# Performance work log

Measured on AMD Instinct MI355X. Metric: run time of the kernel, lower is better.

## Reference

```python
import jax, jax.numpy as jnp
import numpy as np

E = 1024
H = 16          # num_heads
D = E // H      # head_dim
HID = 1024      # hidden_dim
B, S = 16, 512
EPS = 1e-5


def _ln(x, g, b):
    mu = jnp.mean(x, axis=-1, keepdims=True)
    var = jnp.mean(jnp.square(x - mu), axis=-1, keepdims=True)
    return (x - mu) * jax.lax.rsqrt(var + EPS) * g + b


def setup_inputs() -> dict:
    key = jax.random.key(0)
    ks = jax.random.split(key, 8)
    s = 1.0 / np.sqrt(E)
    return {
        'state_features': jax.random.normal(ks[0], (6, B, S, E), jnp.float32),
        'Wq': jax.random.normal(ks[1], (E, E), jnp.float32) * s,
        'bq': jnp.zeros((E,), jnp.float32),
        'Wk': jax.random.normal(ks[2], (E, E), jnp.float32) * s,
        'bk': jnp.zeros((E,), jnp.float32),
        'Wv': jax.random.normal(ks[3], (E, E), jnp.float32) * s,
        'bv': jnp.zeros((E,), jnp.float32),
        'Wo': jax.random.normal(ks[4], (E, E), jnp.float32) * s,
        'bo': jnp.zeros((E,), jnp.float32),
        'ln1_g': jnp.ones((E,), jnp.float32),
        'ln1_b': jnp.zeros((E,), jnp.float32),
        'fusion_w': jnp.ones((6,), jnp.float32) / 6.0,
        'Wf': jax.random.normal(ks[5], (HID, E), jnp.float32) * s,
        'bf': jnp.zeros((HID,), jnp.float32),
        'ln2_g': jnp.ones((HID,), jnp.float32),
        'ln2_b': jnp.zeros((HID,), jnp.float32),
    }


def reference(state_features, Wq, bq, Wk, bk, Wv, bv, Wo, bo,
              ln1_g, ln1_b, fusion_w, Wf, bf, ln2_g, ln2_b):
    # state_features: (6, B, S, E) -> stacked (N, 6, E), N = B*S
    st = jnp.transpose(state_features, (1, 2, 0, 3)).reshape(B * S, 6, E)
    N = st.shape[0]

    q = (st @ Wq.T + bq).reshape(N, 6, H, D)
    k = (st @ Wk.T + bk).reshape(N, 6, H, D)
    v = (st @ Wv.T + bv).reshape(N, 6, H, D)

    # tiny 6x6 attention per token per head (dropout = identity in eval)
    scores = jnp.einsum('nqhd,nkhd->nhqk', q, k) / np.sqrt(D).astype(np.float32)
    attn = jax.nn.softmax(scores, axis=-1)
    ctx = jnp.einsum('nhqk,nkhd->nqhd', attn, v).reshape(N, 6, E)

    out = ctx @ Wo.T + bo
    enhanced = _ln(out + st, ln1_g, ln1_b)  # (N, 6, E)

    # weighted_sum fusion
    w = jax.nn.softmax(fusion_w)
    fused = jnp.einsum('nse,s->ne', enhanced, w)

    hidden = fused @ Wf.T + bf
    hidden = jnp.where(hidden >= 0, hidden, 0.01 * hidden)  # LeakyReLU(0.01)
    hidden = _ln(hidden, ln2_g, ln2_b)
    return hidden.reshape(B, S, HID)
```

## Files before the change

### kernel.cpp

```cpp
#include <hip/hip_runtime.h>
#include <hip/hip_bf16.h>

#define NTOK 8192
#define E 1024
#define NS 6
#define MBIG (NTOK * NS)
#define NSE ((long)NTOK * E)

typedef short short8 __attribute__((ext_vector_type(8)));
typedef float f32x4 __attribute__((ext_vector_type(4)));
typedef unsigned short ushort4v __attribute__((ext_vector_type(4)));

#define TM 128
#define TN 128
#define BK 64

static __device__ __forceinline__ float bf2f(unsigned short u) {
    union { unsigned int i; float f; } c; c.i = ((unsigned int)u) << 16; return c.f;
}

struct WPtrs { const float* s[5]; __hip_bfloat16* d[5]; };
__global__ __launch_bounds__(256) void cvt5_w(WPtrs p)
{
    const int seg = blockIdx.x >> 10;
    const int i = ((blockIdx.x & 1023) * 256 + threadIdx.x) * 4;
    const float4 v = *(const float4*)(p.s[seg] + i);
    union { __hip_bfloat16 h[4]; unsigned long long u; } pk;
    pk.h[0] = (__hip_bfloat16)v.x;
    pk.h[1] = (__hip_bfloat16)v.y;
    pk.h[2] = (__hip_bfloat16)v.z;
    pk.h[3] = (__hip_bfloat16)v.w;
    *(unsigned long long*)(p.d[seg] + i) = pk.u;
}

__global__ __launch_bounds__(256) void cvt_bulk(
    const float* __restrict__ src, __hip_bfloat16* __restrict__ dst)
{
    const long i = ((long)blockIdx.x * 256 + threadIdx.x) * 4;
    const float4 v = *(const float4*)(src + i);
    union { __hip_bfloat16 h[4]; unsigned long long u; } pk;
    pk.h[0] = (__hip_bfloat16)v.x;
    pk.h[1] = (__hip_bfloat16)v.y;
    pk.h[2] = (__hip_bfloat16)v.z;
    pk.h[3] = (__hip_bfloat16)v.w;
    *(unsigned long long*)(dst + i) = pk.u;
}

#define KTILES 16
#define NITER  8

static __device__ __forceinline__ void stage_half(
    const __hip_bfloat16* gsrc,
    __hip_bfloat16* ldst, int tid)
{
#pragma unroll
    for (int piece = 0; piece < 2; ++piece) {
        const int r  = piece * 64 + (tid >> 3);
        const int s  = tid & 7;
        const int ss = s ^ (r & 7);
        const __hip_bfloat16* g = gsrc + (long)r * 1024 + ss * 8;
        __hip_bfloat16* l = ldst + r * 64 + s * 8;
        __builtin_amdgcn_global_load_lds((const __attribute__((address_space(1))) void*)g,
                                         (__attribute__((address_space(3))) void*)l, 16, 0, 0);
    }
}

static __device__ __forceinline__ short8 ld_frag(
    const __hip_bfloat16* half_base, int lr, int slot)
{
    return *(const short8*)(half_base + lr * 64 + ((slot ^ (lr & 7)) << 3));
}

#define STAGE(kt, part)                                                         \
  {                                                                             \
    const int _b  = (kt) & 1;                                                   \
    const int _ab = (part) >> 1;                                                \
    const int _hf = (part) & 1;                                                 \
    const __hip_bfloat16* _g = (_ab == 0)                                       \
        ? A  + (m0 + _hf * 128) * 1024 + (kt) * 64                              \
        : Wb + ((long)n0 + _hf * 128) * 1024 + (kt) * 64;                       \
    stage_half(_g, &lds[((_b * 2 + _ab) * 2 + _hf) * 8192], tid);               \
  }

#define PHASE(kt, q, STMT_STAGE, STMT_WAIT)                                     \
  {                                                                             \
    const int _buf = (kt) & 1;                                                  \
    const __hip_bfloat16* _Ab = &lds[((_buf * 2 + 0) * 2 + wm) * 8192];         \
    const __hip_bfloat16* _Bb = &lds[((_buf * 2 + 1) * 2 + (wn >> 1)) * 8192];  \
    if ((q) == 0) {                                                             \
      _Pragma("unroll") for (int nf = 0; nf < 4; ++nf)                          \
        _Pragma("unroll") for (int k2 = 0; k2 < 2; ++k2)                        \
          bfr[nf][k2] = ld_frag(_Bb, (wn & 1) * 64 + nf * 16 + mrow,            \
                                k2 * 4 + quad);                                 \
    }                                                                           \
    _Pragma("unroll") for (int mf = 0; mf < 2; ++mf)                            \
      _Pragma("unroll") for (int k2 = 0; k2 < 2; ++k2)                          \
        afr[mf][k2] = ld_frag(_Ab, (q) * 32 + mf * 16 + mrow, k2 * 4 + quad);   \
    STMT_STAGE;                                                                 \
    STMT_WAIT;                                                                  \
    __builtin_amdgcn_s_barrier();                                               \
    asm volatile("s_waitcnt lgkmcnt(0)" ::: "memory");                          \
    __builtin_amdgcn_sched_barrier(0);                                          \
    __builtin_amdgcn_s_setprio(1);                                              \
    _Pragma("unroll") for (int mf = 0; mf < 2; ++mf)                            \
      _Pragma("unroll") for (int nf = 0; nf < 4; ++nf)                          \
        _Pragma("unroll") for (int k2 = 0; k2 < 2; ++k2)                        \
          acc[(q) * 2 + mf][nf] = __builtin_amdgcn_mfma_f32_16x16x32_bf16(      \
              afr[mf][k2], bfr[nf][k2], acc[(q) * 2 + mf][nf], 0, 0, 0);        \
    __builtin_amdgcn_s_setprio(0);                                              \
    __builtin_amdgcn_s_barrier();                                               \
  }

__global__ __launch_bounds__(512) void gemm256(
    const __hip_bfloat16* __restrict__ A,
    const __hip_bfloat16* __restrict__ Wb,
    const float* __restrict__ bias,
    __hip_bfloat16* __restrict__ C)
{
    __shared__ __hip_bfloat16 lds[2 * 2 * 2 * 8192] __attribute__((aligned(16)));

    const int tid  = threadIdx.x;
    const int lane = tid & 63;
    const int wid  = tid >> 6;
    const int quad = lane >> 4;
    const int mrow = lane & 15;
    const int wm = wid >> 2;
    const int wn = wid & 3;

    const int nwg = gridDim.x * gridDim.y;
    const int cpx = nwg >> 3;
    const int lin = blockIdx.y * gridDim.x + blockIdx.x;
    const int tile = (lin & 7) * cpx + (lin >> 3);
    const int  n0 = (tile & 3) * 256;
    const long m0 = (long)(tile >> 2) * 256;

    f32x4 acc[8][4] = {};
    short8 bfr[4][2];
    short8 afr[2][2];

    STAGE(0, 0); STAGE(0, 1); STAGE(0, 2); STAGE(0, 3);
    STAGE(1, 2); STAGE(1, 3);
    asm volatile("s_waitcnt vmcnt(4)" ::: "memory");
    __builtin_amdgcn_s_barrier();

#pragma unroll 1
    for (int it = 0; it < NITER; ++it) {
        const int kt0 = 2 * it;
        const int kt1 = 2 * it + 1;
        const bool more = (it < NITER - 1);

        PHASE(kt0, 0, STAGE(kt1, 0), ((void)0));
        PHASE(kt0, 1, STAGE(kt1, 1), ((void)0));
        PHASE(kt0, 2, if (more) STAGE(kt0 + 2, 2), ((void)0));
        PHASE(kt0, 3, if (more) STAGE(kt0 + 2, 3),
              if (more) { asm volatile("s_waitcnt vmcnt(4)" ::: "memory"); }
              else      { asm volatile("s_waitcnt vmcnt(0)" ::: "memory"); });
        PHASE(kt1, 0, if (more) STAGE(kt0 + 2, 0), ((void)0));
        PHASE(kt1, 1, if (more) STAGE(kt0 + 2, 1), ((void)0));
        PHASE(kt1, 2, if (more) STAGE(kt0 + 3, 2), ((void)0));
        PHASE(kt1, 3, if (more) STAGE(kt0 + 3, 3),
              if (more) { asm volatile("s_waitcnt vmcnt(4)" ::: "memory"); });
    }

#pragma unroll
    for (int mf = 0; mf < 8; ++mf) {
#pragma unroll
        for (int nf = 0; nf < 4; ++nf) {
            const int col = n0 + wn * 64 + nf * 16 + mrow;
            const float bv = bias[col];
#pragma unroll
            for (int r = 0; r < 4; ++r) {
                const long row = m0 + wm * 128 + mf * 16 + quad * 4 + r;
                C[row * 1024 + col] = (__hip_bfloat16)(acc[mf][nf][r] + bv);
            }
        }
    }
}

__global__ __launch_bounds__(256) void gemm_bt(
    const __hip_bfloat16* __restrict__ A,
    const __hip_bfloat16* __restrict__ Wb,
    const float* __restrict__ bias,
    __hip_bfloat16* __restrict__ C)
{
    __shared__ __hip_bfloat16 lA[TM * BK] __attribute__((aligned(16)));
    __shared__ __hip_bfloat16 lB[TN * BK] __attribute__((aligned(16)));

    const int tid  = threadIdx.x;
    const int wave = tid >> 6;
    const int lane = tid & 63;
    const int quad = lane >> 4;
    const int mrow = lane & 15;
    const int wr = wave >> 1;
    const int wc = wave & 1;

    const int Gy   = gridDim.y;
    const int lin  = blockIdx.y * 8 + blockIdx.x;
    const int tile = (lin & 7) * Gy + (lin >> 3);
    const int  n0 = (tile & 7) * TN;
    const long m0 = (long)(tile >> 3) * TM;

    const int srow = lane >> 3;
    const int scol = (lane & 7) * 8;

    f32x4 acc[4][4] = {};

    for (int k0 = 0; k0 < 1024; k0 += BK) {
        __syncthreads();
#pragma unroll
        for (int it = 0; it < 4; ++it) {
            const int chunk = it * 4 + wave;
            const int row   = chunk * 8 + srow;
            const __hip_bfloat16* ga = A + (m0 + row) * 1024 + k0 + scol;
            const __hip_bfloat16* gb = Wb + (long)(n0 + row) * 1024 + k0 + scol;
            __hip_bfloat16* la = lA + row * BK + scol;
            __hip_bfloat16* lb = lB + row * BK + scol;
            __builtin_amdgcn_global_load_lds((const __attribute__((address_space(1))) void*)ga,
                                             (__attribute__((address_space(3))) void*)la, 16, 0, 0);
            __builtin_amdgcn_global_load_lds((const __attribute__((address_space(1))) void*)gb,
                                             (__attribute__((address_space(3))) void*)lb, 16, 0, 0);
        }
        __syncthreads();

#pragma unroll
        for (int kk = 0; kk < BK; kk += 32) {
            short8 af[4], bfrg[4];
#pragma unroll
            for (int i = 0; i < 4; ++i)
                af[i] = *(const short8*)(lA + (wr * 64 + i * 16 + mrow) * BK + kk + quad * 8);
#pragma unroll
            for (int j = 0; j < 4; ++j)
                bfrg[j] = *(const short8*)(lB + (wc * 64 + j * 16 + mrow) * BK + kk + quad * 8);
#pragma unroll
            for (int i = 0; i < 4; ++i)
#pragma unroll
                for (int j = 0; j < 4; ++j)
                    acc[i][j] = __builtin_amdgcn_mfma_f32_16x16x32_bf16(af[i], bfrg[j], acc[i][j], 0, 0, 0);
        }
    }

#pragma unroll
    for (int i = 0; i < 4; ++i) {
#pragma unroll
        for (int j = 0; j < 4; ++j) {
            const int col = n0 + wc * 64 + j * 16 + mrow;
            const float bv = bias[col];
#pragma unroll
            for (int r = 0; r < 4; ++r) {
                const long row = m0 + wr * 64 + i * 16 + quad * 4 + r;
                C[row * 1024 + col] = (__hip_bfloat16)(acc[i][j][r] + bv);
            }
        }
    }
}

__global__ __launch_bounds__(256) void gemm_a32_bt(
    const float* __restrict__ A,
    const __hip_bfloat16* __restrict__ Wb,
    const float* __restrict__ bias,
    __hip_bfloat16* __restrict__ C)
{
    __shared__ __hip_bfloat16 lA[TM * BK] __attribute__((aligned(16)));
    __shared__ __hip_bfloat16 lB[TN * BK] __attribute__((aligned(16)));

    const int tid  = threadIdx.x;
    const int wave = tid >> 6;
    const int lane = tid & 63;
    const int quad = lane >> 4;
    const int mrow = lane & 15;
    const int wr = wave >> 1;
    const int wc = wave & 1;

    const int Gy   = gridDim.y;
    const int lin  = blockIdx.y * 8 + blockIdx.x;
    const int tile = (lin & 7) * Gy + (lin >> 3);
    const int  n0 = (tile & 7) * TN;
    const long m0 = (long)(tile >> 3) * TM;

    const int srow = lane >> 3;
    const int scol = (lane & 7) * 8;

    f32x4 acc[4][4] = {};

    for (int k0 = 0; k0 < 1024; k0 += BK) {
        __syncthreads();
#pragma unroll
        for (int it = 0; it < 4; ++it) {
            const int chunk = it * 4 + wave;
            const int row   = chunk * 8 + srow;
            const __hip_bfloat16* gb = Wb + (long)(n0 + row) * 1024 + k0 + scol;
            __hip_bfloat16* lb = lB + row * BK + scol;
            __builtin_amdgcn_global_load_lds((const __attribute__((address_space(1))) void*)gb,
                                             (__attribute__((address_space(3))) void*)lb, 16, 0, 0);
        }
#pragma unroll
        for (int u = 0; u < 8; ++u) {
            const int c   = u * 256 + tid;
            const int row = c >> 4;
            const int c4  = c & 15;
            const float4 av = *(const float4*)(A + (m0 + row) * 1024 + k0 + c4 * 4);
            union { __hip_bfloat16 h[4]; unsigned long long uu; } pk;
            pk.h[0] = (__hip_bfloat16)av.x;
            pk.h[1] = (__hip_bfloat16)av.y;
            pk.h[2] = (__hip_bfloat16)av.z;
            pk.h[3] = (__hip_bfloat16)av.w;
            *(unsigned long long*)(lA + row * BK + c4 * 4) = pk.uu;
        }
        __syncthreads();

#pragma unroll
        for (int kk = 0; kk < BK; kk += 32) {
            short8 af[4], bfrg[4];
#pragma unroll
            for (int i = 0; i < 4; ++i)
                af[i] = *(const short8*)(lA + (wr * 64 + i * 16 + mrow) * BK + kk + quad * 8);
#pragma unroll
            for (int j = 0; j < 4; ++j)
                bfrg[j] = *(const short8*)(lB + (wc * 64 + j * 16 + mrow) * BK + kk + quad * 8);
#pragma unroll
            for (int i = 0; i < 4; ++i)
#pragma unroll
                for (int j = 0; j < 4; ++j)
                    acc[i][j] = __builtin_amdgcn_mfma_f32_16x16x32_bf16(af[i], bfrg[j], acc[i][j], 0, 0, 0);
        }
    }

#pragma unroll
    for (int i = 0; i < 4; ++i) {
#pragma unroll
        for (int j = 0; j < 4; ++j) {
            const int col = n0 + wc * 64 + j * 16 + mrow;
            const float bv = bias[col];
#pragma unroll
            for (int r = 0; r < 4; ++r) {
                const long row = m0 + wr * 64 + i * 16 + quad * 4 + r;
                C[row * 1024 + col] = (__hip_bfloat16)(acc[i][j][r] + bv);
            }
        }
    }
}

__global__ __launch_bounds__(256) void attn6(
    const __hip_bfloat16* qb,
    const __hip_bfloat16* __restrict__ kb,
    const __hip_bfloat16* __restrict__ vb,
    __hip_bfloat16* ctx)
{
    const int w    = blockIdx.x * 4 + (threadIdx.x >> 6);
    const int lane = threadIdx.x & 63;
    const int n  = w >> 2;
    const int hg = w & 3;
    const int h  = hg * 4 + (lane >> 4);
    const int sub = lane & 15;
    const long base = (long)n * 1024 + h * 64 + sub * 4;

    float qf[NS][4], kf[NS][4], vf[NS][4];
#pragma unroll
    for (int s = 0; s < NS; ++s) {
        const ushort4v qs = *(const ushort4v*)(qb + s * NSE + base);
        const ushort4v ks = *(const ushort4v*)(kb + s * NSE + base);
        const ushort4v vs = *(const ushort4v*)(vb + s * NSE + base);
#pragma unroll
        for (int c = 0; c < 4; ++c) {
            qf[s][c] = bf2f(qs[c]);
            kf[s][c] = bf2f(ks[c]);
            vf[s][c] = bf2f(vs[c]);
        }
    }

    float p[NS][NS];
#pragma unroll
    for (int i = 0; i < NS; ++i)
#pragma unroll
        for (int j = 0; j < NS; ++j) {
            float t = qf[i][0] * kf[j][0];
            t = fmaf(qf[i][1], kf[j][1], t);
            t = fmaf(qf[i][2], kf[j][2], t);
            t = fmaf(qf[i][3], kf[j][3], t);
            t += __shfl_xor(t, 1, 64);
            t += __shfl_xor(t, 2, 64);
            t += __shfl_xor(t, 4, 64);
            t += __shfl_xor(t, 8, 64);
            p[i][j] = t * 0.125f;
        }

#pragma unroll
    for (int i = 0; i < NS; ++i) {
        float m = p[i][0];
#pragma unroll
        for (int j = 1; j < NS; ++j) m = fmaxf(m, p[i][j]);
        float sum = 0.f;
#pragma unroll
        for (int j = 0; j < NS; ++j) { p[i][j] = __expf(p[i][j] - m); sum += p[i][j]; }
        const float inv = 1.0f / sum;
        float a[4] = {0.f, 0.f, 0.f, 0.f};
#pragma unroll
        for (int j = 0; j < NS; ++j)
#pragma unroll
            for (int c = 0; c < 4; ++c) a[c] = fmaf(p[i][j], vf[j][c], a[c]);
        union { __hip_bfloat16 h4[4]; unsigned long long u; } pk;
#pragma unroll
        for (int c = 0; c < 4; ++c) pk.h4[c] = (__hip_bfloat16)(a[c] * inv);
        *(unsigned long long*)(ctx + i * NSE + base) = pk.u;
    }
}

__global__ __launch_bounds__(256) void ln1_fuse(
    const __hip_bfloat16* __restrict__ wo_out,
    const float* __restrict__ sf,
    const float* __restrict__ g,
    const float* __restrict__ b,
    const float* __restrict__ fw,
    __hip_bfloat16* __restrict__ fused)
{
    const int n = blockIdx.x, tid = threadIdx.x;
    const int wave = tid >> 6, lane = tid & 63;

    float w[NS];
    float mx = -1e30f;
#pragma unroll
    for (int s = 0; s < NS; ++s) { w[s] = fw[s]; mx = fmaxf(mx, w[s]); }
    float sw = 0.f;
#pragma unroll
    for (int s = 0; s < NS; ++s) { w[s] = __expf(w[s] - mx); sw += w[s]; }
    const float isw = 1.0f / sw;

    float gv[4], bv[4];
#pragma unroll
    for (int c = 0; c < 4; ++c) {
        const int e = c * 256 + tid;
        gv[c] = g[e];
        bv[c] = b[e];
    }

    __shared__ float red[2][4];
    float accf[4] = {0.f, 0.f, 0.f, 0.f};

    for (int s = 0; s < NS; ++s) {
        float x[4];
        float sum = 0.f, sq = 0.f;
#pragma unroll
        for (int c = 0; c < 4; ++c) {
            const long idx = s * NSE + (long)n * 1024 + c * 256 + tid;
            x[c] = (float)wo_out[idx] + sf[idx];
            sum += x[c];
            sq  += x[c] * x[c];
        }
#pragma unroll
        for (int off = 32; off; off >>= 1) {
            sum += __shfl_xor(sum, off, 64);
            sq  += __shfl_xor(sq,  off, 64);
        }
        if (lane == 0) { red[0][wave] = sum; red[1][wave] = sq; }
        __syncthreads();
        sum = red[0][0] + red[0][1] + red[0][2] + red[0][3];
        sq  = red[1][0] + red[1][1] + red[1][2] + red[1][3];
        __syncthreads();
        const float mu   = sum * (1.0f / 1024.0f);
        const float var  = sq * (1.0f / 1024.0f) - mu * mu;
        const float rstd = rsqrtf(var + 1e-5f);
        const float ws_  = w[s] * isw;
#pragma unroll
        for (int c = 0; c < 4; ++c)
            accf[c] += ws_ * ((x[c] - mu) * rstd * gv[c] + bv[c]);
    }
#pragma unroll
    for (int c = 0; c < 4; ++c)
        fused[(long)n * 1024 + c * 256 + tid] = (__hip_bfloat16)accf[c];
}

__global__ __launch_bounds__(256) void ln2_out(
    const __hip_bfloat16* __restrict__ hidden,
    const float* __restrict__ g,
    const float* __restrict__ b,
    float* __restrict__ out)
{
    const int n = blockIdx.x, tid = threadIdx.x;
    const int wave = tid >> 6, lane = tid & 63;
    __shared__ float red[2][4];

    float x[4];
    float sum = 0.f, sq = 0.f;
#pragma unroll
    for (int c = 0; c < 4; ++c) {
        float t = (float)hidden[(long)n * 1024 + c * 256 + tid];
        t = t >= 0.f ? t : 0.01f * t;
        x[c] = t;
        sum += t;
        sq  += t * t;
    }
#pragma unroll
    for (int off = 32; off; off >>= 1) {
        sum += __shfl_xor(sum, off, 64);
        sq  += __shfl_xor(sq,  off, 64);
    }
    if (lane == 0) { red[0][wave] = sum; red[1][wave] = sq; }
    __syncthreads();
    sum = red[0][0] + red[0][1] + red[0][2] + red[0][3];
    sq  = red[1][0] + red[1][1] + red[1][2] + red[1][3];
    const float mu   = sum * (1.0f / 1024.0f);
    const float var  = sq * (1.0f / 1024.0f) - mu * mu;
    const float rstd = rsqrtf(var + 1e-5f);
#pragma unroll
    for (int c = 0; c < 4; ++c) {
        const int e = c * 256 + tid;
        out[(long)n * 1024 + e] = (x[c] - mu) * rstd * g[e] + b[e];
    }
}

extern "C" void kernel_launch(void* const* d_in, const int* in_sizes, int n_in,
                              void* d_out, int out_size, void* d_ws, size_t ws_size,
                              hipStream_t stream)
{
    const float* SF  = (const float*)d_in[0];
    const float* Wq  = (const float*)d_in[1];
    const float* bq  = (const float*)d_in[2];
    const float* Wk  = (const float*)d_in[3];
    const float* bk  = (const float*)d_in[4];
    const float* Wv  = (const float*)d_in[5];
    const float* bv  = (const float*)d_in[6];
    const float* Wo  = (const float*)d_in[7];
    const float* bo  = (const float*)d_in[8];
    const float* g1  = (const float*)d_in[9];
    const float* b1  = (const float*)d_in[10];
    const float* fw  = (const float*)d_in[11];
    const float* Wf  = (const float*)d_in[12];
    const float* bf_ = (const float*)d_in[13];
    const float* g2  = (const float*)d_in[14];
    const float* b2  = (const float*)d_in[15];
    float* out = (float*)d_out;

    const size_t REG = (size_t)MBIG * 1024 * sizeof(__hip_bfloat16);
    const size_t WTS = (size_t)5 * 1024 * 1024 * sizeof(__hip_bfloat16);
    const bool big_ws = ws_size >= 4 * REG + WTS;

    __hip_bfloat16* r0  = (__hip_bfloat16*)d_ws;
    __hip_bfloat16* r1  = r0 + (long)MBIG * 1024;
    __hip_bfloat16* r2  = r1 + (long)MBIG * 1024;
    __hip_bfloat16* r3  = r2 + (long)MBIG * 1024;
    __hip_bfloat16* wb  = big_ws ? (r3 + (long)MBIG * 1024) : r3;
    __hip_bfloat16* Wqb = wb;
    __hip_bfloat16* Wkb = Wqb + 1024 * 1024;
    __hip_bfloat16* Wvb = Wkb + 1024 * 1024;
    __hip_bfloat16* Wob = Wvb + 1024 * 1024;
    __hip_bfloat16* Wfb = Wob + 1024 * 1024;

    const dim3 blk(256);

    WPtrs wp;
    wp.s[0] = Wq; wp.s[1] = Wk; wp.s[2] = Wv; wp.s[3] = Wo; wp.s[4] = Wf;
    wp.d[0] = Wqb; wp.d[1] = Wkb; wp.d[2] = Wvb; wp.d[3] = Wob; wp.d[4] = Wfb;
    cvt5_w<<<5 * 1024, blk, 0, stream>>>(wp);

    cvt_bulk<<<MBIG, blk, 0, stream>>>(SF, r2);

    if (big_ws) {
        const dim3 blk2(512);
        const dim3 gB2(4, MBIG / 256);
        const dim3 gS2(4, NTOK / 256);

        gemm256<<<gB2, blk2, 0, stream>>>(r2, Wqb, bq, r0);
        gemm256<<<gB2, blk2, 0, stream>>>(r2, Wkb, bk, r1);
        gemm256<<<gB2, blk2, 0, stream>>>(r2, Wvb, bv, r3);

        attn6<<<NTOK, blk, 0, stream>>>(r0, r1, r3, r0);

        gemm256<<<gB2, blk2, 0, stream>>>(r0, Wob, bo, r1);

        ln1_fuse<<<NTOK, blk, 0, stream>>>(r1, SF, g1, b1, fw, r2);

        gemm256<<<gS2, blk2, 0, stream>>>(r2, Wfb, bf_, r0);

        ln2_out<<<NTOK, blk, 0, stream>>>(r0, g2, b2, out);
    } else {
        const dim3 gBig(8, MBIG / TM);
        const dim3 gSm(8, NTOK / TM);

        gemm_bt<<<gBig, blk, 0, stream>>>(r2, Wqb, bq, r0);
        gemm_bt<<<gBig, blk, 0, stream>>>(r2, Wkb, bk, r1);
        gemm_a32_bt<<<gBig, blk, 0, stream>>>(SF, Wvb, bv, r2);
        attn6<<<NTOK, blk, 0, stream>>>(r0, r1, r2, r0);
        gemm_bt<<<gBig, blk, 0, stream>>>(r0, Wob, bo, r1);
        ln1_fuse<<<NTOK, blk, 0, stream>>>(r1, SF, g1, b1, fw, r2);
        gemm_bt<<<gSm, blk, 0, stream>>>(r2, Wfb, bf_, r0);
        ln2_out<<<NTOK, blk, 0, stream>>>(r0, g2, b2, out);
    }
}
```

Measured before the change: 898.1 us.

## Fuse QKV projections into one GEMM launch and vectorize epilogues and LN kernels

Result: slower. 928.3 us (+3.4%).

```diff
diff --git a/kernel.cpp b/kernel.cpp
--- a/kernel.cpp
+++ b/kernel.cpp
@@ -46,8 +46,9 @@
     *(unsigned long long*)(dst + i) = pk.u;
 }
 
-#define KTILES 16
 #define NITER  8
+
+struct GOut { __hip_bfloat16* C[3]; const float* bias[3]; };
 
 static __device__ __forceinline__ void stage_half(
     const __hip_bfloat16* gsrc,
@@ -106,7 +107,7 @@
       _Pragma("unroll") for (int nf = 0; nf < 4; ++nf)                          \
         _Pragma("unroll") for (int k2 = 0; k2 < 2; ++k2)                        \
           acc[(q) * 2 + mf][nf] = __builtin_amdgcn_mfma_f32_16x16x32_bf16(      \
-              afr[mf][k2], bfr[nf][k2], acc[(q) * 2 + mf][nf], 0, 0, 0);        \
+              bfr[nf][k2], afr[mf][k2], acc[(q) * 2 + mf][nf], 0, 0, 0);        \
     __builtin_amdgcn_s_setprio(0);                                              \
     __builtin_amdgcn_s_barrier();                                               \
   }
@@ -114,8 +115,7 @@
 __global__ __launch_bounds__(512) void gemm256(
     const __hip_bfloat16* __restrict__ A,
     const __hip_bfloat16* __restrict__ Wb,
-    const float* __restrict__ bias,
-    __hip_bfloat16* __restrict__ C)
+    GOut out)
 {
     __shared__ __hip_bfloat16 lds[2 * 2 * 2 * 8192] __attribute__((aligned(16)));
 
@@ -127,12 +127,13 @@
     const int wm = wid >> 2;
     const int wn = wid & 3;
 
-    const int nwg = gridDim.x * gridDim.y;
+    const int gx  = gridDim.x;
+    const int nwg = gx * gridDim.y;
     const int cpx = nwg >> 3;
-    const int lin = blockIdx.y * gridDim.x + blockIdx.x;
+    const int lin = blockIdx.y * gx + blockIdx.x;
     const int tile = (lin & 7) * cpx + (lin >> 3);
-    const int  n0 = (tile & 3) * 256;
-    const long m0 = (long)(tile >> 2) * 256;
+    const int  n0 = (tile % gx) * 256;
+    const long m0 = (long)(tile / gx) * 256;
 
     f32x4 acc[8][4] = {};
     short8 bfr[4][2];
@@ -162,17 +163,22 @@
               if (more) { asm volatile("s_waitcnt vmcnt(4)" ::: "memory"); });
     }
 
+    const int seg = n0 >> 10;
+    const int nb  = n0 & 1023;
+    __hip_bfloat16* Cp = out.C[seg];
+    const float* bp = out.bias[seg];
 #pragma unroll
     for (int mf = 0; mf < 8; ++mf) {
+        const long row = m0 + wm * 128 + mf * 16 + mrow;
 #pragma unroll
         for (int nf = 0; nf < 4; ++nf) {
-            const int col = n0 + wn * 64 + nf * 16 + mrow;
-            const float bv = bias[col];
-#pragma unroll
-            for (int r = 0; r < 4; ++r) {
-                const long row = m0 + wm * 128 + mf * 16 + quad * 4 + r;
-                C[row * 1024 + col] = (__hip_bfloat16)(acc[mf][nf][r] + bv);
-            }
+            const int colb = nb + wn * 64 + nf * 16 + quad * 4;
+            const f32x4 bv4 = *(const f32x4*)(bp + colb);
+            union { __hip_bfloat16 h[4]; unsigned long long u; } pk;
+#pragma unroll
+            for (int r = 0; r < 4; ++r)
+                pk.h[r] = (__hip_bfloat16)(acc[mf][nf][r] + bv4[r]);
+            *(unsigned long long*)(Cp + row * 1024 + colb) = pk.u;
         }
     }
 }
@@ -415,6 +421,7 @@
 {
     const int n = blockIdx.x, tid = threadIdx.x;
     const int wave = tid >> 6, lane = tid & 63;
+    const int e0 = tid * 4;
 
     float w[NS];
     float mx = -1e30f;
@@ -425,24 +432,21 @@
     for (int s = 0; s < NS; ++s) { w[s] = __expf(w[s] - mx); sw += w[s]; }
     const float isw = 1.0f / sw;
 
-    float gv[4], bv[4];
-#pragma unroll
-    for (int c = 0; c < 4; ++c) {
-        const int e = c * 256 + tid;
-        gv[c] = g[e];
-        bv[c] = b[e];
-    }
+    const f32x4 gv4 = *(const f32x4*)(g + e0);
+    const f32x4 bv4 = *(const f32x4*)(b + e0);
 
     __shared__ float red[2][4];
     float accf[4] = {0.f, 0.f, 0.f, 0.f};
 
     for (int s = 0; s < NS; ++s) {
+        const long base = s * NSE + (long)n * 1024 + e0;
+        const ushort4v wv = *(const ushort4v*)(wo_out + base);
+        const f32x4   sv = *(const f32x4*)(sf + base);
         float x[4];
         float sum = 0.f, sq = 0.f;
 #pragma unroll
         for (int c = 0; c < 4; ++c) {
-            const long idx = s * NSE + (long)n * 1024 + c * 256 + tid;
-            x[c] = (float)wo_out[idx] + sf[idx];
+            x[c] = bf2f(wv[c]) + sv[c];
             sum += x[c];
             sq  += x[c] * x[c];
         }
@@ -462,11 +466,12 @@
         const float ws_  = w[s] * isw;
 #pragma unroll
         for (int c = 0; c < 4; ++c)
-            accf[c] += ws_ * ((x[c] - mu) * rstd * gv[c] + bv[c]);
-    }
-#pragma unroll
-    for (int c = 0; c < 4; ++c)
-        fused[(long)n * 1024 + c * 256 + tid] = (__hip_bfloat16)accf[c];
+            accf[c] += ws_ * ((x[c] - mu) * rstd * gv4[c] + bv4[c]);
+    }
+    union { __hip_bfloat16 h4[4]; unsigned long long u; } pk;
+#pragma unroll
+    for (int c = 0; c < 4; ++c) pk.h4[c] = (__hip_bfloat16)accf[c];
+    *(unsigned long long*)(fused + (long)n * 1024 + e0) = pk.u;
 }
 
 __global__ __launch_bounds__(256) void ln2_out(
@@ -477,13 +482,15 @@
 {
     const int n = blockIdx.x, tid = threadIdx.x;
     const int wave = tid >> 6, lane = tid & 63;
+    const int e0 = tid * 4;
     __shared__ float red[2][4];
 
+    const ushort4v hv = *(const ushort4v*)(hidden + (long)n * 1024 + e0);
     float x[4];
     float sum = 0.f, sq = 0.f;
 #pragma unroll
     for (int c = 0; c < 4; ++c) {
-        float t = (float)hidden[(long)n * 1024 + c * 256 + tid];
+        float t = bf2f(hv[c]);
         t = t >= 0.f ? t : 0.01f * t;
         x[c] = t;
         sum += t;
@@ -501,11 +508,14 @@
     const float mu   = sum * (1.0f / 1024.0f);
     const float var  = sq * (1.0f / 1024.0f) - mu * mu;
     const float rstd = rsqrtf(var + 1e-5f);
-#pragma unroll
-    for (int c = 0; c < 4; ++c) {
-        const int e = c * 256 + tid;
-        out[(long)n * 1024 + e] = (x[c] - mu) * rstd * g[e] + b[e];
-    }
+
+    const f32x4 gv4 = *(const f32x4*)(g + e0);
+    const f32x4 bv4 = *(const f32x4*)(b + e0);
+    f32x4 o;
+#pragma unroll
+    for (int c = 0; c < 4; ++c)
+        o[c] = (x[c] - mu) * rstd * gv4[c] + bv4[c];
+    *(f32x4*)(out + (long)n * 1024 + e0) = o;
 }
 
 extern "C" void kernel_launch(void* const* d_in, const int* in_sizes, int n_in,
@@ -556,20 +566,24 @@
 
     if (big_ws) {
         const dim3 blk2(512);
+        const dim3 gQKV(12, MBIG / 256);
         const dim3 gB2(4, MBIG / 256);
-        const dim3 gS2(4, NTOK / 256);
-
-        gemm256<<<gB2, blk2, 0, stream>>>(r2, Wqb, bq, r0);
-        gemm256<<<gB2, blk2, 0, stream>>>(r2, Wkb, bk, r1);
-        gemm256<<<gB2, blk2, 0, stream>>>(r2, Wvb, bv, r3);
+
+        GOut oqkv;
+        oqkv.C[0] = r0; oqkv.C[1] = r1; oqkv.C[2] = r3;
+        oqkv.bias[0] = bq; oqkv.bias[1] = bk; oqkv.bias[2] = bv;
+        gemm256<<<gQKV, blk2, 0, stream>>>(r2, Wqb, oqkv);
 
         attn6<<<NTOK, blk, 0, stream>>>(r0, r1, r3, r0);
 
-        gemm256<<<gB2, blk2, 0, stream>>>(r0, Wob, bo, r1);
+        GOut owo;
+        owo.C[0] = r1; owo.C[1] = r1; owo.C[2] = r1;
+        owo.bias[0] = bo; owo.bias[1] = bo; owo.bias[2] = bo;
+        gemm256<<<gB2, blk2, 0, stream>>>(r0, Wob, owo);
 
         ln1_fuse<<<NTOK, blk, 0, stream>>>(r1, SF, g1, b1, fw, r2);
 
-        gemm256<<<gS2, blk2, 0, stream>>>(r2, Wfb, bf_, r0);
+        gemm_bt<<<dim3(8, NTOK / TM), blk, 0, stream>>>(r2, Wfb, bf_, r0);
 
         ln2_out<<<NTOK, blk, 0, stream>>>(r0, g2, b2, out);
     } else {
```
